# Performance work log

Measured on AMD Instinct MI355X. Metric: run time of the kernel, lower is better.

The kernel has to match this reference:

```python
import jax, jax.numpy as jnp
import numpy as np

B, S, IN, H, OUT = 64, 2048, 256, 128, 3


def setup_inputs() -> dict:
    key = jax.random.key(0)
    ks = jax.random.split(key, 7)
    s_in = 1.0 / np.sqrt(IN)
    s_h = 1.0 / np.sqrt(H)
    return {
        "x": jax.random.normal(ks[0], (B, S, IN), dtype=jnp.float32),
        "W_xh": jax.random.uniform(ks[1], (H, IN), jnp.float32, -s_in, s_in),
        "b_xh": jax.random.uniform(ks[2], (H,), jnp.float32, -s_in, s_in),
        "W_hh": jax.random.uniform(ks[3], (H, H), jnp.float32, -s_h, s_h),
        "b_hh": jax.random.uniform(ks[4], (H,), jnp.float32, -s_h, s_h),
        "b_h": jnp.zeros((H,), dtype=jnp.float32),
        "W_fc": jax.random.uniform(ks[5], (OUT, H), jnp.float32, -s_h, s_h),
        "b_fc": jax.random.uniform(ks[6], (OUT,), jnp.float32, -s_h, s_h),
    }


def reference(x, W_xh, b_xh, W_hh, b_hh, b_h, W_fc, b_fc):
    batch = x.shape[0]
    hidden = W_hh.shape[0]
    # Precompute input projection for all timesteps in one batched matmul: [B,S,H]
    xproj = jnp.einsum("bsi,hi->bsh", x, W_xh) + b_xh
    bias = b_hh + b_h  # fused constant bias per step

    def step(h, xp_t):
        # h: [B,H], xp_t: [B,H]
        h_new = jnp.tanh(xp_t + h @ W_hh.T + bias)
        return h_new, None

    h0 = jnp.zeros((batch, hidden), dtype=x.dtype)
    h_final, _ = jax.lax.scan(step, h0, jnp.swapaxes(xproj, 0, 1))  # scan over S
    return h_final @ W_fc.T + b_fc
```

## Files before the change

### kernel.cpp

```cpp
#include <hip/hip_runtime.h>
#include <hip/hip_bf16.h>
#include <hip/hip_fp16.h>


#define RNN_B   64
#define RNN_S   2048
#define RNN_IN  256
#define RNN_H   128
#define RNN_OUT 3

typedef _Float16 half2v __attribute__((ext_vector_type(2)));
typedef _Float16 half4 __attribute__((ext_vector_type(4)));
typedef _Float16 half8 __attribute__((ext_vector_type(8)));
typedef float f32x4 __attribute__((ext_vector_type(4)));

#if __has_builtin(__builtin_amdgcn_fdot2)
#define FDOT2(a, b, c) __builtin_amdgcn_fdot2((a), (b), (c), false)
#else
#define FDOT2(a, b, c) \
  fmaf((float)(a).x, (float)(b).x, fmaf((float)(a).y, (float)(b).y, (c)))
#endif

#define HPOSH(k) (40 * ((k) >> 5) + ((k) & 31))

__global__ __launch_bounds__(256) void xproj_mfma(
    const float* __restrict__ x, const float* __restrict__ Wxh,
    const float* __restrict__ bxh, float* __restrict__ xp) {
  __shared__ __align__(16) _Float16 Ash[128][40];
  __shared__ __align__(16) _Float16 Bsh[128][40];

  const int tid = threadIdx.x;
  const int m0 = blockIdx.x * 128;
  const int wv = tid >> 6;
  const int lane = tid & 63;
  const int wr = wv >> 1;
  const int wc = wv & 1;
  const int fr = lane & 15;
  const int fk = lane >> 4;

  const int lr = tid >> 3;
  const int lc = (tid & 7) * 4;

  f32x4 acc[4][4];
#pragma unroll
  for (int m = 0; m < 4; ++m)
#pragma unroll
    for (int n = 0; n < 4; ++n) {
      acc[m][n][0] = 0.f; acc[m][n][1] = 0.f;
      acc[m][n][2] = 0.f; acc[m][n][3] = 0.f;
    }

  for (int kc = 0; kc < RNN_IN; kc += 32) {
#pragma unroll
    for (int p = 0; p < 4; ++p) {
      const int row = lr + 32 * p;
      const float4 va = *(const float4*)&x[(size_t)(m0 + row) * RNN_IN + kc + lc];
      half4 ha;
      ha.x = (_Float16)va.x; ha.y = (_Float16)va.y;
      ha.z = (_Float16)va.z; ha.w = (_Float16)va.w;
      *(half4*)&Ash[row][lc] = ha;
      const float4 vb = *(const float4*)&Wxh[(size_t)row * RNN_IN + kc + lc];
      half4 hb;
      hb.x = (_Float16)vb.x; hb.y = (_Float16)vb.y;
      hb.z = (_Float16)vb.z; hb.w = (_Float16)vb.w;
      *(half4*)&Bsh[row][lc] = hb;
    }
    __syncthreads();

    half8 af[4], bf[4];
#pragma unroll
    for (int m = 0; m < 4; ++m)
      af[m] = *(const half8*)&Ash[wr * 64 + m * 16 + fr][fk * 8];
#pragma unroll
    for (int n = 0; n < 4; ++n)
      bf[n] = *(const half8*)&Bsh[wc * 64 + n * 16 + fr][fk * 8];
#pragma unroll
    for (int m = 0; m < 4; ++m)
#pragma unroll
      for (int n = 0; n < 4; ++n)
        acc[m][n] = __builtin_amdgcn_mfma_f32_16x16x32_f16(
            af[m], bf[n], acc[m][n], 0, 0, 0);
    __syncthreads();
  }

  float bb[4];
#pragma unroll
  for (int n = 0; n < 4; ++n) bb[n] = bxh[wc * 64 + n * 16 + fr];
#pragma unroll
  for (int m = 0; m < 4; ++m) {
    const size_t rbase = (size_t)(m0 + wr * 64 + m * 16 + 4 * fk);
#pragma unroll
    for (int reg = 0; reg < 4; ++reg) {
      float* rowp = &xp[(rbase + reg) * RNN_H];
#pragma unroll
      for (int n = 0; n < 4; ++n)
        rowp[wc * 64 + n * 16 + fr] = acc[m][n][reg] + bb[n];
    }
  }
}

__device__ __forceinline__ float fast_tanh(float a) {
  const float e = __expf(2.f * a);
  return 1.f - 2.f / (e + 1.f);
}

__device__ __forceinline__ void block_sync_lds() {
  asm volatile("s_waitcnt lgkmcnt(0)" ::: "memory");
  __builtin_amdgcn_s_barrier();
}

__device__ __forceinline__ float quad_sum_dpp(float s) {
  int t = __builtin_amdgcn_mov_dpp(__builtin_bit_cast(int, s),
                                   0xB1, 0xF, 0xF, true);
  s += __builtin_bit_cast(float, t);
  t = __builtin_amdgcn_mov_dpp(__builtin_bit_cast(int, s),
                               0x4E, 0xF, 0xF, true);
  s += __builtin_bit_cast(float, t);
  return s;
}

#define RNN_W_LIST(M) \
  M(0)  M(1)  M(2)  M(3)  M(4)  M(5)  M(6)  M(7)  \
  M(8)  M(9)  M(10) M(11) M(12) M(13) M(14) M(15)

#define WDECL(i) half2v w##i;
#define WLOADH(i)                                   \
  {                                                 \
    half2v _t;                                      \
    _t.x = (_Float16)wr[2 * (i)];                   \
    _t.y = (_Float16)wr[2 * (i) + 1];               \
    w##i = _t;                                      \
  }

#define RNN_STEP(BIN, BOUT, PREG, TNEXT)                              \
  {                                                                  \
    const float4* hq = (const float4*)(BIN) + 5 * q;                 \
    const float xin = PREG;                                          \
    PREG = xpb[(size_t)(TNEXT) * RNN_H + r];                         \
    union { float4 f4; half2v h[4]; } u0, u1, u2, u3;                \
    u0.f4 = hq[0]; u1.f4 = hq[1]; u2.f4 = hq[2]; u3.f4 = hq[3];      \
    float acc0 = 0.f, acc1 = 0.f, acc2 = 0.f, acc3 = 0.f;            \
    acc0 = FDOT2(w0,  u0.h[0], acc0);                                \
    acc1 = FDOT2(w1,  u0.h[1], acc1);                                \
    acc2 = FDOT2(w2,  u0.h[2], acc2);                                \
    acc3 = FDOT2(w3,  u0.h[3], acc3);                                \
    acc0 = FDOT2(w4,  u1.h[0], acc0);                                \
    acc1 = FDOT2(w5,  u1.h[1], acc1);                                \
    acc2 = FDOT2(w6,  u1.h[2], acc2);                                \
    acc3 = FDOT2(w7,  u1.h[3], acc3);                                \
    acc0 = FDOT2(w8,  u2.h[0], acc0);                                \
    acc1 = FDOT2(w9,  u2.h[1], acc1);                                \
    acc2 = FDOT2(w10, u2.h[2], acc2);                                \
    acc3 = FDOT2(w11, u2.h[3], acc3);                                \
    acc0 = FDOT2(w12, u3.h[0], acc0);                                \
    acc1 = FDOT2(w13, u3.h[1], acc1);                                \
    acc2 = FDOT2(w14, u3.h[2], acc2);                                \
    acc3 = FDOT2(w15, u3.h[3], acc3);                                \
    float s = (acc0 + acc1) + (acc2 + acc3);                         \
    s = quad_sum_dpp(s);                                             \
    const float hv = fast_tanh(bias + xin + s);                      \
    if (q == 0) ((_Float16*)(BOUT))[hw] = (_Float16)hv;              \
    block_sync_lds();                                                \
  }

__global__ __launch_bounds__(512, 2) void rnn_scan(
    const float* __restrict__ xp, const float* __restrict__ Whh,
    const float* __restrict__ bhh, const float* __restrict__ bh,
    const float* __restrict__ Wfc, const float* __restrict__ bfc,
    float* __restrict__ out) {
  const int b = blockIdx.x;
  const int tid = threadIdx.x;
  const int wv = tid >> 6;
  const int lane = tid & 63;
  const int q = lane & 3;
  const int r = wv * 16 + (lane >> 2);

  __shared__ float4 hsA[20];
  __shared__ float4 hsB[20];

  const float* wr = &Whh[(size_t)r * RNN_H + 32 * q];
  RNN_W_LIST(WDECL)
  RNN_W_LIST(WLOADH)

  const float bias = bhh[r] + bh[r];
  const int hw = HPOSH(r);

  if (tid < 80) ((float*)hsA)[tid] = 0.f;
  block_sync_lds();

  const float* xpb = xp + (size_t)b * RNN_S * RNN_H;

  float p0 = xpb[0 * RNN_H + r];
  float p1 = xpb[1 * RNN_H + r];
  float p2 = xpb[2 * RNN_H + r];
  float p3 = xpb[3 * RNN_H + r];

#pragma unroll 1
  for (int t = 0; t < RNN_S; t += 4) {
    const int n0 = (t + 4 < RNN_S) ? t + 4 : RNN_S - 1;
    const int n1 = (t + 5 < RNN_S) ? t + 5 : RNN_S - 1;
    const int n2 = (t + 6 < RNN_S) ? t + 6 : RNN_S - 1;
    const int n3 = (t + 7 < RNN_S) ? t + 7 : RNN_S - 1;
    RNN_STEP(hsA, hsB, p0, n0)
    RNN_STEP(hsB, hsA, p1, n1)
    RNN_STEP(hsA, hsB, p2, n2)
    RNN_STEP(hsB, hsA, p3, n3)
  }

  if (tid < RNN_OUT) {
    float s = bfc[tid];
    const _Float16* hf = (const _Float16*)hsA;
#pragma unroll 4
    for (int k = 0; k < RNN_H; ++k)
      s = fmaf(Wfc[(size_t)tid * RNN_H + k], (float)hf[HPOSH(k)], s);
    out[b * RNN_OUT + tid] = s;
  }
}

extern "C" void kernel_launch(void* const* d_in, const int* in_sizes, int n_in,
                              void* d_out, int out_size, void* d_ws, size_t ws_size,
                              hipStream_t stream) {
  const float* x   = (const float*)d_in[0];
  const float* Wxh = (const float*)d_in[1];
  const float* bxh = (const float*)d_in[2];
  const float* Whh = (const float*)d_in[3];
  const float* bhh = (const float*)d_in[4];
  const float* bh  = (const float*)d_in[5];
  const float* Wfc = (const float*)d_in[6];
  const float* bfc = (const float*)d_in[7];
  float* out = (float*)d_out;
  float* xp  = (float*)d_ws;

  xproj_mfma<<<dim3((RNN_B * RNN_S) / 128), dim3(256), 0, stream>>>(x, Wxh, bxh, xp);
  rnn_scan<<<dim3(RNN_B), dim3(512), 0, stream>>>(xp, Whh, bhh, bh, Wfc, bfc, out);
}
```

Baseline: 790.2 us.

## Run recurrent scan in a single wavefront per batch to drop block barriers

The recurrent scan now runs with one 64-lane wavefront per batch element instead of eight wavefronts. Each lane owns two hidden rows and keeps their full fp16 weight rows in registers, so it computes whole dot products without the cross-lane DPP reduction. Because only one wave touches the shared hidden state, the per-step block barrier becomes a plain LDS wait, and a single buffer replaces the double buffer. In exchange, each lane does eight times more dot-product work per step on one SIMD, and register pressure rises to about 128 VGPRs for the weights. The final FC layer becomes a per-lane partial product followed by a small shared-memory reduction.

Measured after the change: 1.155 ms. +46.2%, slower.

```diff
diff --git a/kernel.cpp b/kernel.cpp
--- a/kernel.cpp
+++ b/kernel.cpp
@@ -20,8 +20,6 @@
 #define FDOT2(a, b, c) \
   fmaf((float)(a).x, (float)(b).x, fmaf((float)(a).y, (float)(b).y, (c)))
 #endif
-
-#define HPOSH(k) (40 * ((k) >> 5) + ((k) & 31))
 
 __global__ __launch_bounds__(256) void xproj_mfma(
     const float* __restrict__ x, const float* __restrict__ Wxh,
@@ -104,96 +102,76 @@
   return 1.f - 2.f / (e + 1.f);
 }
 
-__device__ __forceinline__ void block_sync_lds() {
-  asm volatile("s_waitcnt lgkmcnt(0)" ::: "memory");
-  __builtin_amdgcn_s_barrier();
-}
-
-__device__ __forceinline__ float quad_sum_dpp(float s) {
-  int t = __builtin_amdgcn_mov_dpp(__builtin_bit_cast(int, s),
-                                   0xB1, 0xF, 0xF, true);
-  s += __builtin_bit_cast(float, t);
-  t = __builtin_amdgcn_mov_dpp(__builtin_bit_cast(int, s),
-                               0x4E, 0xF, 0xF, true);
-  s += __builtin_bit_cast(float, t);
-  return s;
-}
-
-#define RNN_W_LIST(M) \
-  M(0)  M(1)  M(2)  M(3)  M(4)  M(5)  M(6)  M(7)  \
-  M(8)  M(9)  M(10) M(11) M(12) M(13) M(14) M(15)
-
-#define WDECL(i) half2v w##i;
-#define WLOADH(i)                                   \
-  {                                                 \
-    half2v _t;                                      \
-    _t.x = (_Float16)wr[2 * (i)];                   \
-    _t.y = (_Float16)wr[2 * (i) + 1];               \
-    w##i = _t;                                      \
-  }
-
-#define RNN_STEP(BIN, BOUT, PREG, TNEXT)                              \
-  {                                                                  \
-    const float4* hq = (const float4*)(BIN) + 5 * q;                 \
-    const float xin = PREG;                                          \
-    PREG = xpb[(size_t)(TNEXT) * RNN_H + r];                         \
-    union { float4 f4; half2v h[4]; } u0, u1, u2, u3;                \
-    u0.f4 = hq[0]; u1.f4 = hq[1]; u2.f4 = hq[2]; u3.f4 = hq[3];      \
-    float acc0 = 0.f, acc1 = 0.f, acc2 = 0.f, acc3 = 0.f;            \
-    acc0 = FDOT2(w0,  u0.h[0], acc0);                                \
-    acc1 = FDOT2(w1,  u0.h[1], acc1);                                \
-    acc2 = FDOT2(w2,  u0.h[2], acc2);                                \
-    acc3 = FDOT2(w3,  u0.h[3], acc3);                                \
-    acc0 = FDOT2(w4,  u1.h[0], acc0);                                \
-    acc1 = FDOT2(w5,  u1.h[1], acc1);                                \
-    acc2 = FDOT2(w6,  u1.h[2], acc2);                                \
-    acc3 = FDOT2(w7,  u1.h[3], acc3);                                \
-    acc0 = FDOT2(w8,  u2.h[0], acc0);                                \
-    acc1 = FDOT2(w9,  u2.h[1], acc1);                                \
-    acc2 = FDOT2(w10, u2.h[2], acc2);                                \
-    acc3 = FDOT2(w11, u2.h[3], acc3);                                \
-    acc0 = FDOT2(w12, u3.h[0], acc0);                                \
-    acc1 = FDOT2(w13, u3.h[1], acc1);                                \
-    acc2 = FDOT2(w14, u3.h[2], acc2);                                \
-    acc3 = FDOT2(w15, u3.h[3], acc3);                                \
-    float s = (acc0 + acc1) + (acc2 + acc3);                         \
-    s = quad_sum_dpp(s);                                             \
-    const float hv = fast_tanh(bias + xin + s);                      \
-    if (q == 0) ((_Float16*)(BOUT))[hw] = (_Float16)hv;              \
-    block_sync_lds();                                                \
-  }
-
-__global__ __launch_bounds__(512, 2) void rnn_scan(
+
+#define RNN_STEP1(PREG, TNEXT)                                        \
+  {                                                                   \
+    const float xin0 = PREG.x, xin1 = PREG.y;                         \
+    PREG = *(const float2*)&xpb[(size_t)(TNEXT) * RNN_H];             \
+    float accA[4] = {0.f, 0.f, 0.f, 0.f};                             \
+    float accB[4] = {0.f, 0.f, 0.f, 0.f};                             \
+    const float4* hv4 = (const float4*)hs;                            \
+    _Pragma("unroll")                                                 \
+    for (int c = 0; c < 4; ++c) {                                     \
+      union { float4 f4[4]; half2v h[16]; } u;                        \
+      u.f4[0] = hv4[4 * c + 0];                                       \
+      u.f4[1] = hv4[4 * c + 1];                                       \
+      u.f4[2] = hv4[4 * c + 2];                                       \
+      u.f4[3] = hv4[4 * c + 3];                                       \
+      _Pragma("unroll")                                               \
+      for (int i = 0; i < 16; ++i) {                                  \
+        accA[i & 3] = FDOT2(wA[16 * c + i], u.h[i], accA[i & 3]);     \
+        accB[i & 3] = FDOT2(wB[16 * c + i], u.h[i], accB[i & 3]);     \
+      }                                                               \
+    }                                                                 \
+    const float sA = (accA[0] + accA[1]) + (accA[2] + accA[3]);       \
+    const float sB = (accB[0] + accB[1]) + (accB[2] + accB[3]);       \
+    hfA = fast_tanh(biasA + xin0 + sA);                               \
+    hfB = fast_tanh(biasB + xin1 + sB);                               \
+    half2v hn;                                                        \
+    hn.x = (_Float16)hfA;                                             \
+    hn.y = (_Float16)hfB;                                             \
+    *(half2v*)&hs[2 * j] = hn;                                        \
+    asm volatile("s_waitcnt lgkmcnt(0)" ::: "memory");                \
+  }
+
+__global__ __launch_bounds__(64) void rnn_scan(
     const float* __restrict__ xp, const float* __restrict__ Whh,
     const float* __restrict__ bhh, const float* __restrict__ bh,
     const float* __restrict__ Wfc, const float* __restrict__ bfc,
     float* __restrict__ out) {
   const int b = blockIdx.x;
-  const int tid = threadIdx.x;
-  const int wv = tid >> 6;
-  const int lane = tid & 63;
-  const int q = lane & 3;
-  const int r = wv * 16 + (lane >> 2);
-
-  __shared__ float4 hsA[20];
-  __shared__ float4 hsB[20];
-
-  const float* wr = &Whh[(size_t)r * RNN_H + 32 * q];
-  RNN_W_LIST(WDECL)
-  RNN_W_LIST(WLOADH)
-
-  const float bias = bhh[r] + bh[r];
-  const int hw = HPOSH(r);
-
-  if (tid < 80) ((float*)hsA)[tid] = 0.f;
-  block_sync_lds();
-
-  const float* xpb = xp + (size_t)b * RNN_S * RNN_H;
-
-  float p0 = xpb[0 * RNN_H + r];
-  float p1 = xpb[1 * RNN_H + r];
-  float p2 = xpb[2 * RNN_H + r];
-  float p3 = xpb[3 * RNN_H + r];
+  const int j = threadIdx.x;
+
+  __shared__ __align__(16) _Float16 hs[RNN_H];
+  __shared__ float fcred[RNN_OUT][64];
+
+  half2v wA[64], wB[64];
+  const float* rowA = &Whh[(size_t)(2 * j) * RNN_H];
+  const float* rowB = rowA + RNN_H;
+#pragma unroll
+  for (int i = 0; i < 32; ++i) {
+    const float4 fa = *(const float4*)&rowA[4 * i];
+    const float4 fb = *(const float4*)&rowB[4 * i];
+    half2v t0; t0.x = (_Float16)fa.x; t0.y = (_Float16)fa.y; wA[2 * i] = t0;
+    half2v t1; t1.x = (_Float16)fa.z; t1.y = (_Float16)fa.w; wA[2 * i + 1] = t1;
+    half2v s0; s0.x = (_Float16)fb.x; s0.y = (_Float16)fb.y; wB[2 * i] = s0;
+    half2v s1; s1.x = (_Float16)fb.z; s1.y = (_Float16)fb.w; wB[2 * i + 1] = s1;
+  }
+
+  const float biasA = bhh[2 * j] + bh[2 * j];
+  const float biasB = bhh[2 * j + 1] + bh[2 * j + 1];
+
+  ((float*)hs)[j] = 0.f;
+  asm volatile("s_waitcnt lgkmcnt(0)" ::: "memory");
+
+  const float* xpb = xp + (size_t)b * RNN_S * RNN_H + 2 * j;
+
+  float2 p0 = *(const float2*)&xpb[0 * RNN_H];
+  float2 p1 = *(const float2*)&xpb[1 * RNN_H];
+  float2 p2 = *(const float2*)&xpb[2 * RNN_H];
+  float2 p3 = *(const float2*)&xpb[3 * RNN_H];
+
+  float hfA = 0.f, hfB = 0.f;
 
 #pragma unroll 1
   for (int t = 0; t < RNN_S; t += 4) {
@@ -201,19 +179,23 @@
     const int n1 = (t + 5 < RNN_S) ? t + 5 : RNN_S - 1;
     const int n2 = (t + 6 < RNN_S) ? t + 6 : RNN_S - 1;
     const int n3 = (t + 7 < RNN_S) ? t + 7 : RNN_S - 1;
-    RNN_STEP(hsA, hsB, p0, n0)
-    RNN_STEP(hsB, hsA, p1, n1)
-    RNN_STEP(hsA, hsB, p2, n2)
-    RNN_STEP(hsB, hsA, p3, n3)
-  }
-
-  if (tid < RNN_OUT) {
-    float s = bfc[tid];
-    const _Float16* hf = (const _Float16*)hsA;
-#pragma unroll 4
-    for (int k = 0; k < RNN_H; ++k)
-      s = fmaf(Wfc[(size_t)tid * RNN_H + k], (float)hf[HPOSH(k)], s);
-    out[b * RNN_OUT + tid] = s;
+    RNN_STEP1(p0, n0)
+    RNN_STEP1(p1, n1)
+    RNN_STEP1(p2, n2)
+    RNN_STEP1(p3, n3)
+  }
+
+#pragma unroll
+  for (int o = 0; o < RNN_OUT; ++o) {
+    const float2 wf = *(const float2*)&Wfc[(size_t)o * RNN_H + 2 * j];
+    fcred[o][j] = wf.x * hfA + wf.y * hfB;
+  }
+  asm volatile("s_waitcnt lgkmcnt(0)" ::: "memory");
+  if (j < RNN_OUT) {
+    float s = bfc[j];
+#pragma unroll 8
+    for (int k = 0; k < 64; ++k) s += fcred[j][k];
+    out[b * RNN_OUT + j] = s;
   }
 }
 
@@ -232,5 +214,5 @@
   float* xp  = (float*)d_ws;
 
   xproj_mfma<<<dim3((RNN_B * RNN_S) / 128), dim3(256), 0, stream>>>(x, Wxh, bxh, xp);
-  rnn_scan<<<dim3(RNN_B), dim3(512), 0, stream>>>(xp, Whh, bhh, bh, Wfc, bfc, out);
-}
+  rnn_scan<<<dim3(RNN_B), dim3(64), 0, stream>>>(xp, Whh, bhh, bh, Wfc, bfc, out);
+}
```
